# Performance work log

Measured on AMD Instinct MI355X. Metric: run time of the kernel, lower is better.

Reference implementation:

```python
import jax, jax.numpy as jnp
import numpy as np

DEC_HIDDEN = 512


def setup_inputs() -> dict:
    key = jax.random.key(0)
    k1, k2, k3, k4 = jax.random.split(key, 4)
    B, S, DEC, ENC2 = 32, 2048, 512, 1024
    s = jax.random.normal(k1, (1, B, DEC), dtype=jnp.float32)
    enc_output = jax.random.normal(k2, (B, S, ENC2), dtype=jnp.float32)
    # nn.Linear weights: attn [dec_hidden, enc_hidden*2 + dec_hidden], v [1, dec_hidden]
    W_attn = jax.random.normal(k3, (DEC, DEC + ENC2), dtype=jnp.float32) * (1.0 / np.sqrt(DEC + ENC2))
    W_v = jax.random.normal(k4, (1, DEC), dtype=jnp.float32) * (1.0 / np.sqrt(DEC))
    return {"s": s, "enc_output": enc_output, "W_attn": W_attn, "W_v": W_v}


def reference(s, enc_output, W_attn, W_v):
    # s: [1, B, D] -> [B, D]; enc_output: [B, S, 2E]
    s = jnp.squeeze(s, axis=0)
    dec = s.shape[-1]
    # torch.cat((s_repeated, enc_output), dim=2) @ W_attn.T, computed without
    # materializing the repeat/concat: split W_attn by column blocks.
    W_s = W_attn[:, :dec]       # [D, D]   (columns matching s)
    W_e = W_attn[:, dec:]       # [D, 2E]  (columns matching enc_output)
    # energy: [B, S, D]
    energy = jnp.tanh(
        jnp.einsum('bd,hd->bh', s, W_s)[:, None, :]
        + jnp.einsum('bse,he->bsh', enc_output, W_e)
    )
    # atten: [B, S]
    atten = jnp.einsum('bsh,h->bs', energy, W_v[0])
    soft_attn_weights = jax.nn.softmax(atten, axis=1)
    # context: [B, 2E]
    context = jnp.einsum('bs,bse->be', soft_attn_weights, enc_output)
    return (context, soft_attn_weights)
```

## Files before the change

kernel.cpp:

```cpp
#include <hip/hip_runtime.h>
#include <hip/hip_bf16.h>


typedef __attribute__((ext_vector_type(8))) short bf16x8;
typedef __attribute__((ext_vector_type(4))) float f32x4;

#define SB0() __builtin_amdgcn_sched_barrier(0)

static __device__ __forceinline__ unsigned short f2bf(float f) {
    union { float f; unsigned u; } v; v.f = f;
    unsigned r = (v.u + 0x7fffu + ((v.u >> 16) & 1u)) >> 16;
    return (unsigned short)r;
}

static __device__ __forceinline__ unsigned pk2(float x, float y) {
    union { __hip_bfloat162 h; unsigned u; } c;
    c.h = __float22bfloat162_rn(make_float2(x, y));
    return c.u;
}

static __device__ __forceinline__ float fast_tanh(float x) {
    return 1.0f - 2.0f / (__expf(2.0f * x) + 1.0f);
}

__global__ __launch_bounds__(256) void prep_sw(const float* __restrict__ s,
                                               const float* __restrict__ Wat,
                                               float* __restrict__ sW) {
    int id = blockIdx.x * 256 + threadIdx.x;
    int b = id >> 9, h = id & 511;
    const float4* wr = (const float4*)(Wat + (size_t)h * 1536);
    const float4* sr = (const float4*)(s + (size_t)b * 512);
    float acc = 0.f;
#pragma unroll 8
    for (int i = 0; i < 128; ++i) {
        float4 w = wr[i], sv = sr[i];
        acc += w.x * sv.x + w.y * sv.y + w.z * sv.z + w.w * sv.w;
    }
    sW[id] = acc;
}

__global__ __launch_bounds__(256) void prep_weB(const float* __restrict__ Wat,
                                                unsigned short* __restrict__ WebfB) {
    int tid = blockIdx.x * 256 + threadIdx.x;
    int lane = tid & 63;
    int g = tid >> 6;
    int nf = g & 7, step = (g >> 3) & 31, cg = g >> 8;
    int col = cg * 128 + nf * 16 + (lane & 15);
    int k0 = step * 32 + (lane >> 4) * 8;
    const float* src = Wat + (size_t)col * 1536 + 512 + k0;
    float4 w0 = *(const float4*)src;
    float4 w1 = *(const float4*)(src + 4);
    union { unsigned short us[8]; int4 v; } p;
    p.us[0] = f2bf(w0.x); p.us[1] = f2bf(w0.y); p.us[2] = f2bf(w0.z); p.us[3] = f2bf(w0.w);
    p.us[4] = f2bf(w1.x); p.us[5] = f2bf(w1.y); p.us[6] = f2bf(w1.z); p.us[7] = f2bf(w1.w);
    *(int4*)(WebfB + (size_t)tid * 8) = p.v;
}

__global__ __launch_bounds__(256, 3) void energy_kernel(
    const float* __restrict__ enc, const unsigned short* __restrict__ WebfB,
    const float* __restrict__ sW, const float* __restrict__ Wv,
    float* __restrict__ attpart) {
    __shared__ __align__(16) unsigned short lA[2][8192];
    __shared__ float lred[4][64];

    const int t = threadIdx.x;
    const int lane = t & 63;
    const int wave = t >> 6;
    const int rg = wave >> 1;
    const int cgw = wave & 1;
    const int bid = blockIdx.x;
    const int ct = (bid >> 3) & 3;
    const int rt = ((bid >> 5) << 3) | (bid & 7);
    const int m0 = rt * 128;
    const int b = m0 >> 11;
    const int l15 = lane & 15;
    const int lkg = lane >> 4;

    const float* abase = enc + (size_t)m0 * 1024 + (t >> 4) * 1024 + (t & 15) * 4;
    const int wlo = (t >> 4) * 128 + (((t & 15) * 8) ^ (((t >> 4) & 7) << 4));
    const int rbase0 = (rg * 64 + l15) * 128 + ((lkg ^ (l15 & 7)) << 4);
    const int rbase1 = rbase0 ^ 64;

    const unsigned short* wB = WebfB + (size_t)ct * 131072 + lane * 8;

    f32x4 acc[4][4];
#pragma unroll
    for (int mf = 0; mf < 4; ++mf)
#pragma unroll
        for (int nf = 0; nf < 4; ++nf) acc[mf][nf] = (f32x4){0.f, 0.f, 0.f, 0.f};

    float4 areg[8];
    auto load8 = [&](int step) {
#pragma unroll
        for (int q = 0; q < 8; ++q)
            areg[q] = *(const float4*)(abase + q * 16384 + step * 64);
    };
    auto cvtwrite = [&](unsigned short* buf) {
        char* base = (char*)buf + wlo;
#pragma unroll
        for (int q = 0; q < 8; ++q) {
            uint2 w;
            w.x = pk2(areg[q].x, areg[q].y);
            w.y = pk2(areg[q].z, areg[q].w);
            *(uint2*)(base + q * 2048) = w;
        }
    };
    bf16x8 bfr[8];
    auto loadB = [&](int i) {
#pragma unroll
        for (int kk = 0; kk < 2; ++kk)
#pragma unroll
            for (int nf = 0; nf < 4; ++nf)
                bfr[kk * 4 + nf] = *(const bf16x8*)(
                    wB + (((size_t)((i * 2 + kk) * 8 + cgw * 4 + nf)) << 9));
    };
    auto compute = [&](const unsigned short* buf) {
#pragma unroll
        for (int kk = 0; kk < 2; ++kk) {
            const int rb = kk ? rbase1 : rbase0;
#pragma unroll
            for (int mf = 0; mf < 4; ++mf) {
                bf16x8 af = *(const bf16x8*)((const char*)buf + rb + mf * 2048);
#pragma unroll
                for (int nf = 0; nf < 4; ++nf)
                    acc[mf][nf] = __builtin_amdgcn_mfma_f32_16x16x32_bf16(
                        af, bfr[kk * 4 + nf], acc[mf][nf], 0, 0, 0);
            }
        }
    };

    unsigned short* cur = lA[0];
    unsigned short* nxt = lA[1];

    load8(0);
    cvtwrite(cur);
    load8(1);
    asm volatile("s_waitcnt lgkmcnt(0)" ::: "memory");
    __builtin_amdgcn_s_barrier();

#pragma unroll 2
    for (int i = 0; i < 16; ++i) {
        loadB(i);
        SB0();
        if (i < 15) cvtwrite(nxt);
        SB0();
        if (i < 14) load8(i + 2);
        SB0();
        compute(cur);
        asm volatile("s_waitcnt lgkmcnt(0)" ::: "memory");
        SB0();
        __builtin_amdgcn_s_barrier();
        { unsigned short* tp = cur; cur = nxt; nxt = tp; }
    }

    float sWv[4], wvv[4];
#pragma unroll
    for (int nf = 0; nf < 4; ++nf) {
        int col = ct * 128 + cgw * 64 + nf * 16 + l15;
        sWv[nf] = sW[(b << 9) + col];
        wvv[nf] = Wv[col];
    }
    float pa[4][4];
#pragma unroll
    for (int mf = 0; mf < 4; ++mf) {
#pragma unroll
        for (int r = 0; r < 4; ++r) pa[mf][r] = 0.f;
#pragma unroll
        for (int nf = 0; nf < 4; ++nf)
#pragma unroll
            for (int r = 0; r < 4; ++r)
                pa[mf][r] += fast_tanh(acc[mf][nf][r] + sWv[nf]) * wvv[nf];
    }
#pragma unroll
    for (int m = 1; m < 16; m <<= 1)
#pragma unroll
        for (int mf = 0; mf < 4; ++mf)
#pragma unroll
            for (int r = 0; r < 4; ++r)
                pa[mf][r] += __shfl_xor(pa[mf][r], m, 64);

    if (l15 == 0) {
#pragma unroll
        for (int mf = 0; mf < 4; ++mf)
#pragma unroll
            for (int r = 0; r < 4; ++r)
                lred[wave][mf * 16 + lkg * 4 + r] = pa[mf][r];
    }
    __syncthreads();
    if (t < 128) {
        int rgw = t >> 6, rl = t & 63;
        attpart[(size_t)ct * 65536 + m0 + t] =
            lred[rgw * 2 + 0][rl] + lred[rgw * 2 + 1][rl];
    }
}

__global__ __launch_bounds__(256) void softmax_kernel(const float* __restrict__ attpart,
                                                      float* __restrict__ out) {
    int b = blockIdx.x, t = threadIdx.x;
    float v[8];
#pragma unroll
    for (int i = 0; i < 8; ++i) {
        int idx = b * 2048 + t + 256 * i;
        v[i] = ((attpart[idx] + attpart[65536 + idx]) + attpart[131072 + idx])
               + attpart[196608 + idx];
    }
    float mx = v[0];
#pragma unroll
    for (int i = 1; i < 8; ++i) mx = fmaxf(mx, v[i]);
#pragma unroll
    for (int m = 1; m < 64; m <<= 1) mx = fmaxf(mx, __shfl_xor(mx, m, 64));
    __shared__ float redm[4], reds[4];
    if ((t & 63) == 0) redm[t >> 6] = mx;
    __syncthreads();
    mx = fmaxf(fmaxf(redm[0], redm[1]), fmaxf(redm[2], redm[3]));
    float sum = 0.f;
#pragma unroll
    for (int i = 0; i < 8; ++i) { v[i] = __expf(v[i] - mx); sum += v[i]; }
#pragma unroll
    for (int m = 1; m < 64; m <<= 1) sum += __shfl_xor(sum, m, 64);
    if ((t & 63) == 0) reds[t >> 6] = sum;
    __syncthreads();
    sum = reds[0] + reds[1] + reds[2] + reds[3];
    float inv = 1.0f / sum;
    float* soft = out + 32768;
#pragma unroll
    for (int i = 0; i < 8; ++i) soft[b * 2048 + t + 256 * i] = v[i] * inv;
}

__global__ __launch_bounds__(256) void ctx_partial(const float* __restrict__ enc,
                                                   const float* __restrict__ soft,
                                                   float* __restrict__ part) {
    int blk = blockIdx.x;
    int b = blk >> 4, s0 = (blk & 15) * 128;
    int t = threadIdx.x;
    float4 a = {0.f, 0.f, 0.f, 0.f};
    const float* base = enc + ((size_t)(b * 2048 + s0)) * 1024 + t * 4;
    const float* sw = soft + b * 2048 + s0;
#pragma unroll 4
    for (int s = 0; s < 128; ++s) {
        float w = sw[s];
        float4 e = *(const float4*)(base + (size_t)s * 1024);
        a.x += w * e.x; a.y += w * e.y; a.z += w * e.z; a.w += w * e.w;
    }
    *(float4*)(part + (size_t)blk * 1024 + t * 4) = a;
}

__global__ __launch_bounds__(256) void ctx_reduce(const float* __restrict__ part,
                                                  float* __restrict__ ctx) {
    int id = blockIdx.x * 256 + threadIdx.x;
    int b = id >> 10, e = id & 1023;
    float s = 0.f;
#pragma unroll 8
    for (int c = 0; c < 16; ++c) s += part[((size_t)(b * 16 + c)) * 1024 + e];
    ctx[id] = s;
}

extern "C" void kernel_launch(void* const* d_in, const int* in_sizes, int n_in,
                              void* d_out, int out_size, void* d_ws, size_t ws_size,
                              hipStream_t stream) {
    const float* s   = (const float*)d_in[0];
    const float* enc = (const float*)d_in[1];
    const float* Wat = (const float*)d_in[2];
    const float* Wv  = (const float*)d_in[3];
    float* out = (float*)d_out;

    char* ws = (char*)d_ws;
    float* sW             = (float*)ws;
    unsigned short* WebfB = (unsigned short*)(ws + (64 << 10));
    float* attpart        = (float*)(ws + (64 << 10) + (1 << 20));
    float* part           = (float*)(ws + (64 << 10) + (2 << 20));

    prep_sw<<<64, 256, 0, stream>>>(s, Wat, sW);
    prep_weB<<<256, 256, 0, stream>>>(Wat, WebfB);
    energy_kernel<<<2048, 256, 0, stream>>>(enc, WebfB, sW, Wv, attpart);
    softmax_kernel<<<32, 256, 0, stream>>>(attpart, out);
    ctx_partial<<<512, 256, 0, stream>>>(enc, out + 32768, part);
    ctx_reduce<<<128, 256, 0, stream>>>(part, out);
}
```

Measured before the change: 178.1 us.

## Replace LDS-staged energy GEMM with single-wave register-direct MFMA tiles

The energy kernel changes from 256-thread blocks that stage bf16-converted A tiles through double-buffered LDS with barriers, to single-wave 64-thread blocks. Each wave loads fp32 enc rows straight into registers in MFMA fragment order, converts them, and issues MFMAs with a register-level double buffer and s_setprio around the MFMA bursts. The column tile shrinks to 64, giving 8 column tiles, so the B-weight prep layout, the attpart workspace size and the softmax partial-sum loop (now 8 partials) change with it. This removes LDS traffic and block barriers, but each enc row is now re-read by 8 column-tile blocks instead of 4, raising global/L2 traffic on the dominant input.

```diff
diff --git a/kernel.cpp b/kernel.cpp
--- a/kernel.cpp
+++ b/kernel.cpp
@@ -5,7 +5,8 @@
 typedef __attribute__((ext_vector_type(8))) short bf16x8;
 typedef __attribute__((ext_vector_type(4))) float f32x4;
 
-#define SB0() __builtin_amdgcn_sched_barrier(0)
+#define PRIO1 __builtin_amdgcn_s_setprio(1)
+#define PRIO0 __builtin_amdgcn_s_setprio(0)
 
 static __device__ __forceinline__ unsigned short f2bf(float f) {
     union { float f; unsigned u; } v; v.f = f;
@@ -44,9 +45,9 @@
     int tid = blockIdx.x * 256 + threadIdx.x;
     int lane = tid & 63;
     int g = tid >> 6;
-    int nf = g & 7, step = (g >> 3) & 31, cg = g >> 8;
-    int col = cg * 128 + nf * 16 + (lane & 15);
-    int k0 = step * 32 + (lane >> 4) * 8;
+    int nf = g & 3, h = (g >> 2) & 31, ct = g >> 7;
+    int col = ct * 64 + nf * 16 + (lane & 15);
+    int k0 = h * 32 + (lane >> 4) * 8;
     const float* src = Wat + (size_t)col * 1536 + 512 + k0;
     float4 w0 = *(const float4*)src;
     float4 w1 = *(const float4*)(src + 4);
@@ -56,32 +57,25 @@
     *(int4*)(WebfB + (size_t)tid * 8) = p.v;
 }
 
-__global__ __launch_bounds__(256, 3) void energy_kernel(
+__global__ __launch_bounds__(64, 2) void energy_kernel(
     const float* __restrict__ enc, const unsigned short* __restrict__ WebfB,
     const float* __restrict__ sW, const float* __restrict__ Wv,
     float* __restrict__ attpart) {
-    __shared__ __align__(16) unsigned short lA[2][8192];
-    __shared__ float lred[4][64];
-
-    const int t = threadIdx.x;
-    const int lane = t & 63;
-    const int wave = t >> 6;
-    const int rg = wave >> 1;
-    const int cgw = wave & 1;
+    const int lane = threadIdx.x;
     const int bid = blockIdx.x;
-    const int ct = (bid >> 3) & 3;
-    const int rt = ((bid >> 5) << 3) | (bid & 7);
-    const int m0 = rt * 128;
+    const int ct = (bid >> 3) & 7;
+    const int rt = (bid & 7) | ((bid >> 6) << 3);
+    const int m0 = rt * 64;
     const int b = m0 >> 11;
     const int l15 = lane & 15;
     const int lkg = lane >> 4;
 
-    const float* abase = enc + (size_t)m0 * 1024 + (t >> 4) * 1024 + (t & 15) * 4;
-    const int wlo = (t >> 4) * 128 + (((t & 15) * 8) ^ (((t >> 4) & 7) << 4));
-    const int rbase0 = (rg * 64 + l15) * 128 + ((lkg ^ (l15 & 7)) << 4);
-    const int rbase1 = rbase0 ^ 64;
-
-    const unsigned short* wB = WebfB + (size_t)ct * 131072 + lane * 8;
+    const float* abase[4];
+#pragma unroll
+    for (int mf = 0; mf < 4; ++mf)
+        abase[mf] = enc + (size_t)(m0 + mf * 16 + l15) * 1024 + lkg * 8;
+
+    const unsigned short* bb = WebfB + (size_t)ct * 65536 + lane * 8;
 
     f32x4 acc[4][4];
 #pragma unroll
@@ -89,74 +83,57 @@
 #pragma unroll
         for (int nf = 0; nf < 4; ++nf) acc[mf][nf] = (f32x4){0.f, 0.f, 0.f, 0.f};
 
-    float4 areg[8];
-    auto load8 = [&](int step) {
-#pragma unroll
-        for (int q = 0; q < 8; ++q)
-            areg[q] = *(const float4*)(abase + q * 16384 + step * 64);
-    };
-    auto cvtwrite = [&](unsigned short* buf) {
-        char* base = (char*)buf + wlo;
-#pragma unroll
-        for (int q = 0; q < 8; ++q) {
-            uint2 w;
-            w.x = pk2(areg[q].x, areg[q].y);
-            w.y = pk2(areg[q].z, areg[q].w);
-            *(uint2*)(base + q * 2048) = w;
+    float4 a0[8], a1[8];
+    bf16x8 b0[4], b1[4];
+
+    auto LA = [&](float4 (&AZ)[8], int h) {
+#pragma unroll
+        for (int mf = 0; mf < 4; ++mf) {
+            AZ[mf * 2 + 0] = *(const float4*)(abase[mf] + h * 32);
+            AZ[mf * 2 + 1] = *(const float4*)(abase[mf] + h * 32 + 4);
         }
     };
-    bf16x8 bfr[8];
-    auto loadB = [&](int i) {
-#pragma unroll
-        for (int kk = 0; kk < 2; ++kk)
-#pragma unroll
-            for (int nf = 0; nf < 4; ++nf)
-                bfr[kk * 4 + nf] = *(const bf16x8*)(
-                    wB + (((size_t)((i * 2 + kk) * 8 + cgw * 4 + nf)) << 9));
+    auto LB = [&](bf16x8 (&BZ)[4], int h) {
+#pragma unroll
+        for (int nf = 0; nf < 4; ++nf)
+            BZ[nf] = *(const bf16x8*)(bb + (size_t)(h * 4 + nf) * 512);
     };
-    auto compute = [&](const unsigned short* buf) {
-#pragma unroll
-        for (int kk = 0; kk < 2; ++kk) {
-            const int rb = kk ? rbase1 : rbase0;
-#pragma unroll
-            for (int mf = 0; mf < 4; ++mf) {
-                bf16x8 af = *(const bf16x8*)((const char*)buf + rb + mf * 2048);
-#pragma unroll
-                for (int nf = 0; nf < 4; ++nf)
-                    acc[mf][nf] = __builtin_amdgcn_mfma_f32_16x16x32_bf16(
-                        af, bfr[kk * 4 + nf], acc[mf][nf], 0, 0, 0);
-            }
+    auto HALF = [&](float4 (&AZ)[8], bf16x8 (&BZ)[4], int h) {
+        bf16x8 abf[4];
+#pragma unroll
+        for (int mf = 0; mf < 4; ++mf) {
+            union { unsigned u[4]; bf16x8 v; } c;
+            c.u[0] = pk2(AZ[mf * 2].x, AZ[mf * 2].y);
+            c.u[1] = pk2(AZ[mf * 2].z, AZ[mf * 2].w);
+            c.u[2] = pk2(AZ[mf * 2 + 1].x, AZ[mf * 2 + 1].y);
+            c.u[3] = pk2(AZ[mf * 2 + 1].z, AZ[mf * 2 + 1].w);
+            abf[mf] = c.v;
         }
+        if (h + 2 < 32) LA(AZ, h + 2);
+        PRIO1;
+#pragma unroll
+        for (int nf = 0; nf < 4; ++nf)
+#pragma unroll
+            for (int mf = 0; mf < 4; ++mf)
+                acc[mf][nf] = __builtin_amdgcn_mfma_f32_16x16x32_bf16(
+                    abf[mf], BZ[nf], acc[mf][nf], 0, 0, 0);
+        PRIO0;
+        if (h + 2 < 32) LB(BZ, h + 2);
     };
 
-    unsigned short* cur = lA[0];
-    unsigned short* nxt = lA[1];
-
-    load8(0);
-    cvtwrite(cur);
-    load8(1);
-    asm volatile("s_waitcnt lgkmcnt(0)" ::: "memory");
-    __builtin_amdgcn_s_barrier();
-
-#pragma unroll 2
-    for (int i = 0; i < 16; ++i) {
-        loadB(i);
-        SB0();
-        if (i < 15) cvtwrite(nxt);
-        SB0();
-        if (i < 14) load8(i + 2);
-        SB0();
-        compute(cur);
-        asm volatile("s_waitcnt lgkmcnt(0)" ::: "memory");
-        SB0();
-        __builtin_amdgcn_s_barrier();
-        { unsigned short* tp = cur; cur = nxt; nxt = tp; }
+    LA(a0, 0); LB(b0, 0);
+    LA(a1, 1); LB(b1, 1);
+
+#pragma unroll
+    for (int h = 0; h < 32; ++h) {
+        if ((h & 1) == 0) HALF(a0, b0, h);
+        else              HALF(a1, b1, h);
     }
 
     float sWv[4], wvv[4];
 #pragma unroll
     for (int nf = 0; nf < 4; ++nf) {
-        int col = ct * 128 + cgw * 64 + nf * 16 + l15;
+        int col = ct * 64 + nf * 16 + l15;
         sWv[nf] = sW[(b << 9) + col];
         wvv[nf] = Wv[col];
     }
@@ -181,16 +158,10 @@
 
     if (l15 == 0) {
 #pragma unroll
-        for (int mf = 0; mf < 4; ++mf)
-#pragma unroll
-            for (int r = 0; r < 4; ++r)
-                lred[wave][mf * 16 + lkg * 4 + r] = pa[mf][r];
-    }
-    __syncthreads();
-    if (t < 128) {
-        int rgw = t >> 6, rl = t & 63;
-        attpart[(size_t)ct * 65536 + m0 + t] =
-            lred[rgw * 2 + 0][rl] + lred[rgw * 2 + 1][rl];
+        for (int mf = 0; mf < 4; ++mf) {
+            float4 v = make_float4(pa[mf][0], pa[mf][1], pa[mf][2], pa[mf][3]);
+            *(float4*)&attpart[(size_t)ct * 65536 + m0 + mf * 16 + lkg * 4] = v;
+        }
     }
 }
 
@@ -201,8 +172,10 @@
 #pragma unroll
     for (int i = 0; i < 8; ++i) {
         int idx = b * 2048 + t + 256 * i;
-        v[i] = ((attpart[idx] + attpart[65536 + idx]) + attpart[131072 + idx])
-               + attpart[196608 + idx];
+        float s0 = 0.f;
+#pragma unroll
+        for (int c = 0; c < 8; ++c) s0 += attpart[c * 65536 + idx];
+        v[i] = s0;
     }
     float mx = v[0];
 #pragma unroll
@@ -268,11 +241,11 @@
     float* sW             = (float*)ws;
     unsigned short* WebfB = (unsigned short*)(ws + (64 << 10));
     float* attpart        = (float*)(ws + (64 << 10) + (1 << 20));
-    float* part           = (float*)(ws + (64 << 10) + (2 << 20));
+    float* part           = (float*)(ws + (64 << 10) + (3 << 20));
 
     prep_sw<<<64, 256, 0, stream>>>(s, Wat, sW);
     prep_weB<<<256, 256, 0, stream>>>(Wat, WebfB);
-    energy_kernel<<<2048, 256, 0, stream>>>(enc, WebfB, sW, Wv, attpart);
+    energy_kernel<<<8192, 64, 0, stream>>>(enc, WebfB, sW, Wv, attpart);
     softmax_kernel<<<32, 256, 0, stream>>>(attpart, out);
     ctx_partial<<<512, 256, 0, stream>>>(enc, out + 32768, part);
     ctx_reduce<<<128, 256, 0, stream>>>(part, out);
```

Result: slower. 345.9 us (+94.2%).
